# Kernel optimization log

Measured on AMD Instinct MI355X. Metric: run time of the kernel, lower is better.

## Reference

```python
import jax, jax.numpy as jnp
import numpy as np

E = 2048      # embed_dim
H = 16        # num_heads
HD = E // H // 2   # differential head dim = 64
S = 2048      # seq len
B = 1         # batch
DEPTH = 12
LAMBDA_INIT = 0.8 - 0.6 * float(np.exp(-0.3 * DEPTH))
EPS = 1e-5


def setup_inputs() -> dict:
    key = jax.random.key(0)
    ks = jax.random.split(key, 12)
    n = lambda k, shape, s=1.0: (jax.random.normal(k, shape, dtype=jnp.float32) * s)
    return {
        "query": n(ks[0], (S, B, E)),
        "key": n(ks[1], (S, B, E)),
        "value": n(ks[2], (S, B, E)),
        "rel_pos": 0,
        "attn_mask": jnp.zeros((B, S), dtype=jnp.bool_),
        "Wq": n(ks[3], (E, E), 0.02),
        "Wk": n(ks[4], (E, E), 0.02),
        "Wv": n(ks[5], (E, E), 0.02),
        "Wo": n(ks[6], (E, E), 0.02),
        "lq1": n(ks[7], (HD,), 0.1),
        "lk1": n(ks[8], (HD,), 0.1),
        "lq2": n(ks[9], (HD,), 0.1),
        "lk2": n(ks[10], (HD,), 0.1),
        "subln_g": jnp.ones((2 * HD,), dtype=jnp.float32),
    }


def reference(query, key, value, rel_pos, attn_mask,
              Wq, Wk, Wv, Wo, lq1, lk1, lq2, lk2, subln_g):
    # (S,B,E) -> (B,S,E)
    q = jnp.einsum("sbe,fe->bsf", query, Wq)
    k = jnp.einsum("sbe,fe->bsf", key, Wk)
    v = jnp.einsum("sbe,fe->bsf", value, Wv)

    bsz, tgt_len, _ = q.shape
    scaling = HD ** -0.5

    q = q.reshape(bsz, tgt_len, 2 * H, HD).transpose(0, 2, 1, 3) * scaling  # (B,2H,S,hd)
    k = k.reshape(bsz, tgt_len, 2 * H, HD).transpose(0, 2, 1, 3)            # (B,2H,S,hd)
    v = v.reshape(bsz, tgt_len, H, 2 * HD).transpose(0, 2, 1, 3)            # (B,H,S,2hd)

    scores = jnp.einsum("bhqd,bhkd->bhqk", q, k)  # (B,2H,S,S)
    mask = jnp.where(attn_mask[:, None, None, :], -jnp.inf, 0.0).astype(scores.dtype)
    scores = jnp.nan_to_num(scores + mask)  # torch.nan_to_num: nan->0, -inf->finite min

    probs = jax.nn.softmax(scores.astype(jnp.float32), axis=-1).astype(scores.dtype)
    probs = jnp.clip(probs, -1e6, 1e6)  # clamp as in original (dropout is identity in eval)

    lam1 = jnp.exp(jnp.sum(lq1 * lk1))
    lam2 = jnp.exp(jnp.sum(lq2 * lk2))
    lam_full = lam1 - lam2 + LAMBDA_INIT

    probs = probs.reshape(bsz, H, 2, tgt_len, tgt_len)
    diff = probs[:, :, 0] - lam_full * probs[:, :, 1]   # (B,H,S,S)

    attn = jnp.einsum("bhqk,bhkd->bhqd", diff, v)       # (B,H,S,2hd)

    # RMSNorm over last dim with affine weight
    rms = jax.lax.rsqrt(jnp.mean(jnp.square(attn), axis=-1, keepdims=True) + EPS)
    attn = attn * rms * subln_g
    attn = attn * (1.0 - LAMBDA_INIT)

    attn = attn.transpose(0, 2, 1, 3).reshape(bsz, tgt_len, H * 2 * HD)  # (B,S,E)
    attn = attn.transpose(1, 0, 2)                                       # (S,B,E)
    return jnp.einsum("sbe,fe->sbf", attn, Wo)
```

## Files before the change

kernel.cpp:

```cpp
#include <hip/hip_runtime.h>
#include <stdint.h>

#define LAMBDA_INIT_F 0.7836057665f

typedef __bf16 bf16x8 __attribute__((ext_vector_type(8)));
typedef float  f32x4  __attribute__((ext_vector_type(4)));
typedef unsigned short u16x8 __attribute__((ext_vector_type(8)));
typedef unsigned short u16x4 __attribute__((ext_vector_type(4)));
typedef short s16x4 __attribute__((ext_vector_type(4)));

__device__ __forceinline__ unsigned short f2b(float f) {
    union { float f; unsigned u; } v; v.f = f;
    unsigned u = v.u;
    return (unsigned short)((u + 0x7fffu + ((u >> 16) & 1u)) >> 16);
}

#define GLD16(gp, sp) __builtin_amdgcn_global_load_lds( \
    (const __attribute__((address_space(1))) void*)(uintptr_t)(gp), \
    (__attribute__((address_space(3))) void*)(uint32_t)(uintptr_t)(sp), 16, 0, 0)

__global__ __launch_bounds__(64) void lam_kernel(const float* lq1, const float* lk1,
                                                 const float* lq2, const float* lk2, float* out) {
    int t = threadIdx.x;
    float p1 = lq1[t] * lk1[t];
    float p2 = lq2[t] * lk2[t];
    for (int off = 32; off; off >>= 1) { p1 += __shfl_xor(p1, off, 64); p2 += __shfl_xor(p2, off, 64); }
    if (t == 0) out[0] = __expf(p1) - __expf(p2) + LAMBDA_INIT_F;
}

__global__ __launch_bounds__(256) void cvt4(const float* __restrict__ s0, const float* __restrict__ s1,
                                            const float* __restrict__ s2, const float* __restrict__ s3,
                                            unsigned short* __restrict__ d0, unsigned short* __restrict__ d1,
                                            unsigned short* __restrict__ d2, unsigned short* __restrict__ d3) {
    int z = blockIdx.y;
    const float* s = z == 0 ? s0 : z == 1 ? s1 : z == 2 ? s2 : s3;
    unsigned short* d = z == 0 ? d0 : z == 1 ? d1 : z == 2 ? d2 : d3;
    size_t i = ((size_t)blockIdx.x * 256 + threadIdx.x) * 8;
    float4 a = *(const float4*)(s + i);
    float4 b = *(const float4*)(s + i + 4);
    u16x8 o;
    o[0] = f2b(a.x); o[1] = f2b(a.y); o[2] = f2b(a.z); o[3] = f2b(a.w);
    o[4] = f2b(b.x); o[5] = f2b(b.y); o[6] = f2b(b.z); o[7] = f2b(b.w);
    *(u16x8*)(d + i) = o;
}

template <int OUT_BF16, int NT, int DO_VT>
__global__ __launch_bounds__(256, 2) void gemm_bt(const unsigned short* __restrict__ Abase,
                                                  const unsigned short* __restrict__ Bbase,
                                                  void* __restrict__ Cbase,
                                                  unsigned short* __restrict__ VT,
                                                  float alpha0) {
    constexpr int MI = (NT == 128) ? 4 : 2;
    __shared__ __align__(16) unsigned short As[128 * 32];
    __shared__ __align__(16) unsigned short Bs[NT * 32];
    const int tid = threadIdx.x;
    const int w = tid >> 6, lane = tid & 63;
    const int quad = lane >> 4, l16 = lane & 15;
    const int b = blockIdx.z;
    const unsigned short* A = Abase + (size_t)b * 4194304;
    const unsigned short* B = Bbase + (size_t)b * 4194304;
    const float alpha = (b == 0) ? alpha0 : 1.0f;
    const int m0 = blockIdx.y * 128, n0 = blockIdx.x * NT;
    const int wm = (NT == 128) ? (w >> 1) * 64 : w * 32;
    const int wn = (NT == 128) ? (w & 1) * 64 : 0;
    const int sr = lane >> 2;
    const int sc = (((lane & 3) ^ ((lane >> 3) & 3)) * 8);
    const int rsw = ((l16 >> 1) & 3);

    f32x4 zz = {0.f, 0.f, 0.f, 0.f};
    f32x4 acc[MI][4];
#pragma unroll
    for (int i = 0; i < MI; ++i)
#pragma unroll
        for (int jn = 0; jn < 4; ++jn) acc[i][jn] = zz;

    for (int k0 = 0; k0 < 2048; k0 += 32) {
        GLD16(A + (size_t)(m0 + w * 16 + sr) * 2048 + k0 + sc,      &As[(w * 16) * 32]);
        GLD16(A + (size_t)(m0 + 64 + w * 16 + sr) * 2048 + k0 + sc, &As[(64 + w * 16) * 32]);
        if (NT == 128) {
            GLD16(B + (size_t)(n0 + w * 16 + sr) * 2048 + k0 + sc,      &Bs[(w * 16) * 32]);
            GLD16(B + (size_t)(n0 + 64 + w * 16 + sr) * 2048 + k0 + sc, &Bs[(64 + (w * 16)) * 32]);
        } else {
            GLD16(B + (size_t)(n0 + w * 16 + sr) * 2048 + k0 + sc, &Bs[(w * 16) * 32]);
        }
        __syncthreads();
        bf16x8 af[MI], bfr[4];
#pragma unroll
        for (int i = 0; i < MI; ++i) af[i]  = *(const bf16x8*)&As[(wm + i * 16 + l16) * 32 + (quad ^ rsw) * 8];
#pragma unroll
        for (int i = 0; i < 4; ++i)  bfr[i] = *(const bf16x8*)&Bs[(wn + i * 16 + l16) * 32 + (quad ^ rsw) * 8];
#pragma unroll
        for (int i = 0; i < MI; ++i)
#pragma unroll
            for (int jn = 0; jn < 4; ++jn)
                acc[i][jn] = __builtin_amdgcn_mfma_f32_16x16x32_bf16(af[i], bfr[jn], acc[i][jn], 0, 0, 0);
        __syncthreads();
    }

    if (DO_VT && b == 2) {
#pragma unroll
        for (int i = 0; i < MI; ++i)
#pragma unroll
            for (int jn = 0; jn < 4; ++jn) {
                int n = n0 + wn + jn * 16 + l16;
                int m = m0 + wm + i * 16 + quad * 4;
                u16x4 o;
#pragma unroll
                for (int r = 0; r < 4; ++r) o[r] = f2b(acc[i][jn][r]);
                *(u16x4*)&VT[(size_t)n * 2048 + m] = o;
            }
    } else {
#pragma unroll
        for (int i = 0; i < MI; ++i)
#pragma unroll
            for (int jn = 0; jn < 4; ++jn)
#pragma unroll
                for (int r = 0; r < 4; ++r) {
                    int row = m0 + wm + i * 16 + quad * 4 + r;
                    int col = n0 + wn + jn * 16 + l16;
                    float v = acc[i][jn][r] * alpha;
                    if (OUT_BF16)
                        ((unsigned short*)Cbase + (size_t)b * 4194304)[(size_t)row * 2048 + col] = f2b(v);
                    else
                        ((float*)Cbase)[(size_t)row * 2048 + col] = v;
                }
    }
}

__global__ __launch_bounds__(256, 2) void diff_attn(const unsigned short* __restrict__ qb,
                                                    const unsigned short* __restrict__ kb,
                                                    const unsigned short* __restrict__ vt,
                                                    const float* __restrict__ lamp,
                                                    const float* __restrict__ g,
                                                    unsigned short* __restrict__ Aout) {
    __shared__ __align__(16) unsigned short Ks[128 * 128];
    __shared__ __align__(16) unsigned short Vs[128 * 128];
    const int tid = threadIdx.x, w = tid >> 6, lane = tid & 63;
    const int quad = lane >> 4, l16 = lane & 15;
    const int j = blockIdx.y;
    const int q0 = blockIdx.x * 64;
    const float lam = lamp[0];

    bf16x8 qf[2][2];
#pragma unroll
    for (int p = 0; p < 2; ++p)
#pragma unroll
        for (int dh = 0; dh < 2; ++dh)
            qf[p][dh] = *(const bf16x8*)&qb[(size_t)(q0 + w * 16 + l16) * 2048 + j * 128 + p * 64 + dh * 32 + quad * 8];

    f32x4 O[2][8];
#pragma unroll
    for (int p = 0; p < 2; ++p)
#pragma unroll
        for (int i = 0; i < 8; ++i)
#pragma unroll
            for (int r = 0; r < 4; ++r) O[p][i][r] = 0.f;
    float lsum[2] = {0.f, 0.f};

    const int srow = lane >> 4;

    for (int kv0 = 0; kv0 < 2048; kv0 += 128) {
#pragma unroll
        for (int t = 0; t < 8; ++t) {
            int rb = (w * 8 + t) * 4;
            int row = rb + srow;
            int cbs = (((lane & 15) ^ (row & 15)) * 8);
            GLD16(kb + (size_t)(kv0 + row) * 2048 + j * 128 + cbs, &Ks[rb * 128]);
            GLD16(vt + (size_t)(j * 128 + row) * 2048 + kv0 + cbs, &Vs[rb * 128]);
        }
        __syncthreads();

        s16x4 pf[2][8];
#pragma unroll
        for (int p = 0; p < 2; ++p) {
#pragma unroll
            for (int i = 0; i < 8; ++i) {
                bf16x8 a0 = *(const bf16x8*)&Ks[(i * 16 + l16) * 128 + ((p * 8 + quad) ^ l16) * 8];
                bf16x8 a1 = *(const bf16x8*)&Ks[(i * 16 + l16) * 128 + ((p * 8 + 4 + quad) ^ l16) * 8];
                f32x4 s = {0.f, 0.f, 0.f, 0.f};
                s = __builtin_amdgcn_mfma_f32_16x16x32_bf16(a0, qf[p][0], s, 0, 0, 0);
                s = __builtin_amdgcn_mfma_f32_16x16x32_bf16(a1, qf[p][1], s, 0, 0, 0);
                float e0 = __expf(s[0]), e1 = __expf(s[1]), e2 = __expf(s[2]), e3 = __expf(s[3]);
                lsum[p] += (e0 + e1) + (e2 + e3);
                s16x4 pv;
                pv[0] = (short)f2b(e0); pv[1] = (short)f2b(e1);
                pv[2] = (short)f2b(e2); pv[3] = (short)f2b(e3);
                pf[p][i] = pv;
            }
        }
#pragma unroll
        for (int i = 0; i < 8; ++i) {
#pragma unroll
            for (int dt = 0; dt < 8; ++dt) {
                int blk = (i * 2 + (quad >> 1)) ^ l16;
                s16x4 vf = *(const s16x4*)&Vs[(dt * 16 + l16) * 128 + blk * 8 + (quad & 1) * 4];
                O[0][dt] = __builtin_amdgcn_mfma_f32_16x16x16bf16_1k(vf, pf[0][i], O[0][dt], 0, 0, 0);
                O[1][dt] = __builtin_amdgcn_mfma_f32_16x16x16bf16_1k(vf, pf[1][i], O[1][dt], 0, 0, 0);
            }
        }
        __syncthreads();
    }

#pragma unroll
    for (int p = 0; p < 2; ++p) {
        lsum[p] += __shfl_xor(lsum[p], 16, 64);
        lsum[p] += __shfl_xor(lsum[p], 32, 64);
    }
    const float inv1 = 1.0f / lsum[0];
    const float inv2 = lam / lsum[1];

    float ssum = 0.f;
#pragma unroll
    for (int dt = 0; dt < 8; ++dt)
#pragma unroll
        for (int r = 0; r < 4; ++r) {
            float v = O[0][dt][r] * inv1 - O[1][dt][r] * inv2;
            O[0][dt][r] = v;
            ssum += v * v;
        }
    ssum += __shfl_xor(ssum, 16, 64);
    ssum += __shfl_xor(ssum, 32, 64);
    const float rms = rsqrtf(ssum * (1.0f / 128.0f) + 1e-5f) * (1.0f - LAMBDA_INIT_F);

#pragma unroll
    for (int dt = 0; dt < 8; ++dt) {
        float4 g4 = *(const float4*)&g[dt * 16 + quad * 4];
        u16x4 o;
        o[0] = f2b(O[0][dt][0] * rms * g4.x);
        o[1] = f2b(O[0][dt][1] * rms * g4.y);
        o[2] = f2b(O[0][dt][2] * rms * g4.z);
        o[3] = f2b(O[0][dt][3] * rms * g4.w);
        *(u16x4*)&Aout[(size_t)(q0 + w * 16 + l16) * 2048 + j * 128 + dt * 16 + quad * 4] = o;
    }
}

extern "C" void kernel_launch(void* const* d_in, const int* in_sizes, int n_in,
                              void* d_out, int out_size, void* d_ws, size_t ws_size,
                              hipStream_t stream) {
    const float* query = (const float*)d_in[0];
    const float* key   = (const float*)d_in[1];
    const float* value = (const float*)d_in[2];
    const float* Wq  = (const float*)d_in[5];
    const float* Wk  = (const float*)d_in[6];
    const float* Wv  = (const float*)d_in[7];
    const float* Wo  = (const float*)d_in[8];
    const float* lq1 = (const float*)d_in[9];
    const float* lk1 = (const float*)d_in[10];
    const float* lq2 = (const float*)d_in[11];
    const float* lk2 = (const float*)d_in[12];
    const float* g   = (const float*)d_in[13];

    char* ws = (char*)d_ws;
    const size_t MB = 1ull << 20;
    const size_t N4 = 4194304;
    unsigned short* qb  = (unsigned short*)(ws + 0 * MB);
    unsigned short* vt  = (unsigned short*)(ws + 16 * MB);
    unsigned short* Aat = (unsigned short*)(ws + 24 * MB);
    unsigned short* Xq  = (unsigned short*)(ws + 32 * MB);
    unsigned short* Wqb = (unsigned short*)(ws + 64 * MB);
    float* lamp = (float*)(ws + 96 * MB);

    lam_kernel<<<dim3(1), dim3(64), 0, stream>>>(lq1, lk1, lq2, lk2, lamp);
    cvt4<<<dim3(2048, 3), dim3(256), 0, stream>>>(query, key, value, value,
                                                  Xq, Xq + N4, Xq + 2 * N4, Xq + 2 * N4);
    cvt4<<<dim3(2048, 4), dim3(256), 0, stream>>>(Wq, Wk, Wv, Wo,
                                                  Wqb, Wqb + N4, Wqb + 2 * N4, Wqb + 3 * N4);
    gemm_bt<1, 128, 1><<<dim3(16, 16, 3), dim3(256), 0, stream>>>(Xq, Wqb, (void*)qb, vt, 0.125f);
    diff_attn<<<dim3(32, 16), dim3(256), 0, stream>>>(qb, qb + N4, vt, lamp, g, Aat);
    gemm_bt<0, 64, 0><<<dim3(32, 16, 1), dim3(256), 0, stream>>>(Aat, Wqb + 3 * N4, d_out, nullptr, 1.0f);
}
```

Before: 339.3 us.

## Merge conversion launches, fold lambda into attention, use exp2 with log2e-scaled Q

The two fp32-to-bf16 conversion launches become one seven-slice launch writing into a contiguous workspace. The lambda computation moves into the attention kernel, which removes a separate launch. The 1/ln2 factor is folded into the Q scaling so the softmax can use the hardware exp2, and bf16 packing uses a cheaper round-half-up perm instead of round-to-nearest-even. QKV GEMM launch bounds are raised to 3 waves per SIMD, which changes rounding slightly and may pressure registers.

```diff
diff --git a/kernel.cpp b/kernel.cpp
--- a/kernel.cpp
+++ b/kernel.cpp
@@ -15,26 +15,32 @@
     return (unsigned short)((u + 0x7fffu + ((u >> 16) & 1u)) >> 16);
 }
 
+__device__ __forceinline__ unsigned pk2(float a, float b) {
+    unsigned ua = __float_as_uint(a) + 0x8000u;
+    unsigned ub = __float_as_uint(b) + 0x8000u;
+    return __builtin_amdgcn_perm(ub, ua, 0x07060302u);
+}
+
+#if __has_builtin(__builtin_amdgcn_exp2f)
+#define EXP2(x) __builtin_amdgcn_exp2f(x)
+#else
+__device__ __forceinline__ float EXP2(float x) {
+    float r; asm volatile("v_exp_f32 %0, %1\n\ts_nop 1" : "=v"(r) : "v"(x)); return r;
+}
+#endif
+
 #define GLD16(gp, sp) __builtin_amdgcn_global_load_lds( \
     (const __attribute__((address_space(1))) void*)(uintptr_t)(gp), \
     (__attribute__((address_space(3))) void*)(uint32_t)(uintptr_t)(sp), 16, 0, 0)
 
-__global__ __launch_bounds__(64) void lam_kernel(const float* lq1, const float* lk1,
-                                                 const float* lq2, const float* lk2, float* out) {
-    int t = threadIdx.x;
-    float p1 = lq1[t] * lk1[t];
-    float p2 = lq2[t] * lk2[t];
-    for (int off = 32; off; off >>= 1) { p1 += __shfl_xor(p1, off, 64); p2 += __shfl_xor(p2, off, 64); }
-    if (t == 0) out[0] = __expf(p1) - __expf(p2) + LAMBDA_INIT_F;
-}
-
-__global__ __launch_bounds__(256) void cvt4(const float* __restrict__ s0, const float* __restrict__ s1,
+__global__ __launch_bounds__(256) void cvt7(const float* __restrict__ s0, const float* __restrict__ s1,
                                             const float* __restrict__ s2, const float* __restrict__ s3,
-                                            unsigned short* __restrict__ d0, unsigned short* __restrict__ d1,
-                                            unsigned short* __restrict__ d2, unsigned short* __restrict__ d3) {
+                                            const float* __restrict__ s4, const float* __restrict__ s5,
+                                            const float* __restrict__ s6,
+                                            unsigned short* __restrict__ dst) {
     int z = blockIdx.y;
-    const float* s = z == 0 ? s0 : z == 1 ? s1 : z == 2 ? s2 : s3;
-    unsigned short* d = z == 0 ? d0 : z == 1 ? d1 : z == 2 ? d2 : d3;
+    const float* s = z == 0 ? s0 : z == 1 ? s1 : z == 2 ? s2 : z == 3 ? s3 : z == 4 ? s4 : z == 5 ? s5 : s6;
+    unsigned short* d = dst + (size_t)z * 4194304;
     size_t i = ((size_t)blockIdx.x * 256 + threadIdx.x) * 8;
     float4 a = *(const float4*)(s + i);
     float4 b = *(const float4*)(s + i + 4);
@@ -44,12 +50,12 @@
     *(u16x8*)(d + i) = o;
 }
 
-template <int OUT_BF16, int NT, int DO_VT>
-__global__ __launch_bounds__(256, 2) void gemm_bt(const unsigned short* __restrict__ Abase,
-                                                  const unsigned short* __restrict__ Bbase,
-                                                  void* __restrict__ Cbase,
-                                                  unsigned short* __restrict__ VT,
-                                                  float alpha0) {
+template <int OUT_BF16, int NT, int DO_VT, int WPB>
+__global__ __launch_bounds__(256, WPB) void gemm_bt(const unsigned short* __restrict__ Abase,
+                                                    const unsigned short* __restrict__ Bbase,
+                                                    void* __restrict__ Cbase,
+                                                    unsigned short* __restrict__ VT,
+                                                    float alpha0) {
     constexpr int MI = (NT == 128) ? 4 : 2;
     __shared__ __align__(16) unsigned short As[128 * 32];
     __shared__ __align__(16) unsigned short Bs[NT * 32];
@@ -130,16 +136,26 @@
 __global__ __launch_bounds__(256, 2) void diff_attn(const unsigned short* __restrict__ qb,
                                                     const unsigned short* __restrict__ kb,
                                                     const unsigned short* __restrict__ vt,
-                                                    const float* __restrict__ lamp,
+                                                    const float* __restrict__ lq1,
+                                                    const float* __restrict__ lk1,
+                                                    const float* __restrict__ lq2,
+                                                    const float* __restrict__ lk2,
                                                     const float* __restrict__ g,
                                                     unsigned short* __restrict__ Aout) {
     __shared__ __align__(16) unsigned short Ks[128 * 128];
     __shared__ __align__(16) unsigned short Vs[128 * 128];
+    __shared__ float lam_s;
     const int tid = threadIdx.x, w = tid >> 6, lane = tid & 63;
     const int quad = lane >> 4, l16 = lane & 15;
     const int j = blockIdx.y;
     const int q0 = blockIdx.x * 64;
-    const float lam = lamp[0];
+
+    if (tid < 64) {
+        float p1 = lq1[tid] * lk1[tid];
+        float p2 = lq2[tid] * lk2[tid];
+        for (int off = 32; off; off >>= 1) { p1 += __shfl_xor(p1, off, 64); p2 += __shfl_xor(p2, off, 64); }
+        if (tid == 0) lam_s = __expf(p1) - __expf(p2) + LAMBDA_INIT_F;
+    }
 
     bf16x8 qf[2][2];
 #pragma unroll
@@ -180,11 +196,12 @@
                 f32x4 s = {0.f, 0.f, 0.f, 0.f};
                 s = __builtin_amdgcn_mfma_f32_16x16x32_bf16(a0, qf[p][0], s, 0, 0, 0);
                 s = __builtin_amdgcn_mfma_f32_16x16x32_bf16(a1, qf[p][1], s, 0, 0, 0);
-                float e0 = __expf(s[0]), e1 = __expf(s[1]), e2 = __expf(s[2]), e3 = __expf(s[3]);
+                float e0 = EXP2(s[0]), e1 = EXP2(s[1]), e2 = EXP2(s[2]), e3 = EXP2(s[3]);
                 lsum[p] += (e0 + e1) + (e2 + e3);
+                unsigned d0 = pk2(e0, e1), d1 = pk2(e2, e3);
                 s16x4 pv;
-                pv[0] = (short)f2b(e0); pv[1] = (short)f2b(e1);
-                pv[2] = (short)f2b(e2); pv[3] = (short)f2b(e3);
+                pv[0] = (short)(d0 & 0xffff); pv[1] = (short)(d0 >> 16);
+                pv[2] = (short)(d1 & 0xffff); pv[3] = (short)(d1 >> 16);
                 pf[p][i] = pv;
             }
         }
@@ -207,7 +224,7 @@
         lsum[p] += __shfl_xor(lsum[p], 32, 64);
     }
     const float inv1 = 1.0f / lsum[0];
-    const float inv2 = lam / lsum[1];
+    const float inv2 = lam_s / lsum[1];
 
     float ssum = 0.f;
 #pragma unroll
@@ -257,15 +274,13 @@
     unsigned short* vt  = (unsigned short*)(ws + 16 * MB);
     unsigned short* Aat = (unsigned short*)(ws + 24 * MB);
     unsigned short* Xq  = (unsigned short*)(ws + 32 * MB);
-    unsigned short* Wqb = (unsigned short*)(ws + 64 * MB);
     float* lamp = (float*)(ws + 96 * MB);
-
-    lam_kernel<<<dim3(1), dim3(64), 0, stream>>>(lq1, lk1, lq2, lk2, lamp);
-    cvt4<<<dim3(2048, 3), dim3(256), 0, stream>>>(query, key, value, value,
-                                                  Xq, Xq + N4, Xq + 2 * N4, Xq + 2 * N4);
-    cvt4<<<dim3(2048, 4), dim3(256), 0, stream>>>(Wq, Wk, Wv, Wo,
-                                                  Wqb, Wqb + N4, Wqb + 2 * N4, Wqb + 3 * N4);
-    gemm_bt<1, 128, 1><<<dim3(16, 16, 3), dim3(256), 0, stream>>>(Xq, Wqb, (void*)qb, vt, 0.125f);
-    diff_attn<<<dim3(32, 16), dim3(256), 0, stream>>>(qb, qb + N4, vt, lamp, g, Aat);
-    gemm_bt<0, 64, 0><<<dim3(32, 16, 1), dim3(256), 0, stream>>>(Aat, Wqb + 3 * N4, d_out, nullptr, 1.0f);
-}
+    (void)lamp;
+
+    const float alpha_q = 0.125f * 1.44269504f;
+
+    cvt7<<<dim3(2048, 7), dim3(256), 0, stream>>>(query, key, value, Wq, Wk, Wv, Wo, Xq);
+    gemm_bt<1, 128, 1, 3><<<dim3(16, 16, 3), dim3(256), 0, stream>>>(Xq, Xq + 3 * N4, (void*)qb, vt, alpha_q);
+    diff_attn<<<dim3(32, 16), dim3(256), 0, stream>>>(qb, qb + N4, vt, lq1, lk1, lq2, lk2, g, Aat);
+    gemm_bt<0, 64, 0, 2><<<dim3(32, 16, 1), dim3(256), 0, stream>>>(Aat, Xq + 6 * N4, d_out, nullptr, 1.0f);
+}
```

After: 334.6 us. Within noise of the previous version (-1.4%).
